# Kernel optimization log

Hardware: AMD Instinct MI355X
Metric: run time of the kernel (lower is better)

Reference implementation:

```python
import jax, jax.numpy as jnp
import numpy as np

N_NODES = 50000
N_EDGES = 500000
IN_CH = 128
OUT_CH = 128
N_TYPES = 2
NEG_SLOPE = 0.2
EPS = 1e-16


def setup_inputs() -> dict:
    key = jax.random.key(0)
    ks = jax.random.split(key, 8)
    x = jax.random.normal(ks[0], (N_NODES, IN_CH), dtype=jnp.float32)
    edge_index = jax.random.randint(ks[1], (2, N_EDGES), 0, N_NODES, dtype=jnp.int64)
    edge_type = jax.random.randint(ks[2], (N_EDGES,), 0, N_TYPES, dtype=jnp.int64)
    # xavier-uniform-like params
    def xav(k, shape, fan_in, fan_out):
        lim = np.sqrt(6.0 / (fan_in + fan_out)).astype(np.float32)
        return jax.random.uniform(k, shape, jnp.float32, -lim, lim)
    weight = xav(ks[3], (N_TYPES, IN_CH, OUT_CH), IN_CH, OUT_CH)
    att = xav(ks[4], (N_TYPES, 2 * OUT_CH), N_TYPES, 2 * OUT_CH)
    root_w = xav(ks[5], (OUT_CH, IN_CH), IN_CH, OUT_CH)
    lim = 1.0 / np.sqrt(IN_CH)
    root_b = jax.random.uniform(ks[6], (OUT_CH,), jnp.float32, -lim, lim)
    return {"x": x, "edge_index": edge_index, "edge_type": edge_type,
            "weight": weight, "att": att, "root_w": root_w, "root_b": root_b}


def reference(x, edge_index, edge_type, weight, att, root_w, root_b):
    n = x.shape[0]
    src, dst = edge_index[0], edge_index[1]
    # Per-edge transform x[src] @ W[edge_type] == gather from per-type node transforms
    h_all = jnp.einsum('ni,tio->nto', x, weight)          # [N, T, O]
    h_src = h_all[src, edge_type]                          # [E, O]
    h_dst = h_all[dst, edge_type]                          # [E, O]
    a = att[edge_type]                                     # [E, 2O]
    o = h_src.shape[1]
    e = (h_src * a[:, :o]).sum(-1) + (h_dst * a[:, o:]).sum(-1)
    e = jnp.where(e > 0, e, NEG_SLOPE * e)                 # leaky_relu
    # segment softmax over dst (stable: subtract per-segment max)
    seg_max = jax.ops.segment_max(e, dst, num_segments=n)
    ex = jnp.exp(e - seg_max[dst])
    denom = jax.ops.segment_sum(ex, dst, num_segments=n)
    alpha = ex / (denom[dst] + EPS)
    # dropout is identity in eval mode
    msg = h_src * alpha[:, None]
    out = jax.ops.segment_sum(msg, dst, num_segments=n)
    out = out + x @ root_w.T + root_b
    return out
```

## Files before the change

kernel.cpp:

```cpp
#include <hip/hip_runtime.h>
#include <hip/hip_bf16.h>

#define N_NODES 50000
#define N_EDGES 500000
#define IN_CH 128
#define OUT_CH 128
#define N_TYPES 2
#define NEG_SLOPE 0.2f
#define EPS_F 1e-16f

typedef __attribute__((ext_vector_type(8))) short bf16x8;
typedef __attribute__((ext_vector_type(4))) float f32x4;

__device__ __forceinline__ unsigned short bf16_rne(float f) {
    unsigned int u = __float_as_uint(f);
    u += 0x7FFFu + ((u >> 16) & 1u);
    return (unsigned short)(u >> 16);
}
__device__ __forceinline__ float bf16_to_f32(unsigned short h) {
    return __uint_as_float(((unsigned int)h) << 16);
}

__global__ __launch_bounds__(256) void bprep_kernel(
    const float* __restrict__ weight, const float* __restrict__ root_w,
    unsigned short* __restrict__ bt_hi, unsigned short* __restrict__ bt_lo)
{
    int i = blockIdx.x * 256 + threadIdx.x;
    if (i >= 384 * 128) return;
    int n = i >> 7, k = i & 127;
    float v;
    if (n < 256) {
        int t = n >> 7, o = n & 127;
        v = weight[(size_t)t * 16384 + (size_t)k * 128 + o];
    } else {
        v = root_w[(size_t)(n - 256) * 128 + k];
    }
    unsigned short h = bf16_rne(v);
    float lo = v - bf16_to_f32(h);
    bt_hi[i] = h;
    bt_lo[i] = bf16_rne(lo);
}

#define MBLK 391
#define LSWZ(row, col) ((row) * 128 + ((col) ^ (((row) & 7) << 3)))

__global__ __launch_bounds__(256, 2) void mfma_gemm_kernel(
    const float* __restrict__ x,
    const unsigned short* __restrict__ bt_hi,
    const unsigned short* __restrict__ bt_lo,
    const float* __restrict__ root_b,
    float* __restrict__ hall, float* __restrict__ out)
{
    __shared__ unsigned short Ah[128 * 128];
    __shared__ unsigned short Al[128 * 128];

    const int tid = threadIdx.x;
    const int bid = blockIdx.x;
    const int c = bid / MBLK;
    const int m0 = (bid - c * MBLK) * 128;

    {
        const float4* xg = (const float4*)x;
        #pragma unroll
        for (int it = 0; it < 16; ++it) {
            int idx = tid + it * 256;
            int r = idx >> 5, c4 = idx & 31;
            int gn = m0 + r;
            float4 v = make_float4(0.f, 0.f, 0.f, 0.f);
            if (gn < N_NODES) v = xg[(size_t)gn * 32 + c4];
            unsigned short h0 = bf16_rne(v.x), h1 = bf16_rne(v.y),
                           h2 = bf16_rne(v.z), h3 = bf16_rne(v.w);
            ushort4 hh = make_ushort4(h0, h1, h2, h3);
            ushort4 ll = make_ushort4(bf16_rne(v.x - bf16_to_f32(h0)),
                                      bf16_rne(v.y - bf16_to_f32(h1)),
                                      bf16_rne(v.z - bf16_to_f32(h2)),
                                      bf16_rne(v.w - bf16_to_f32(h3)));
            int off = LSWZ(r, c4 * 4);
            *(ushort4*)&Ah[off] = hh;
            *(ushort4*)&Al[off] = ll;
        }
    }
    __syncthreads();

    const int lane = tid & 63;
    const int w = tid >> 6;
    const int mh = (w >> 1) * 64;
    const int nh = (w & 1) * 64;
    const int lr = lane & 15;
    const int lk = (lane >> 4) * 8;

    const unsigned short* bh_base =
        bt_hi + ((size_t)(c * 128 + nh + lr)) * 128 + lk;
    const unsigned short* bl_base =
        bt_lo + ((size_t)(c * 128 + nh + lr)) * 128 + lk;

    f32x4 acc[4][4];
    #pragma unroll
    for (int mi = 0; mi < 4; ++mi)
        #pragma unroll
        for (int ni = 0; ni < 4; ++ni)
            acc[mi][ni] = (f32x4){0.f, 0.f, 0.f, 0.f};

    #pragma unroll
    for (int ks = 0; ks < 4; ++ks) {
        const int ko = ks * 32 + lk;
        bf16x8 bh[4], bl[4];
        #pragma unroll
        for (int ni = 0; ni < 4; ++ni) {
            bh[ni] = *(const bf16x8*)(bh_base + ni * 2048 + ks * 32);
            bl[ni] = *(const bf16x8*)(bl_base + ni * 2048 + ks * 32);
        }
        bf16x8 ah[4], al[4];
        #pragma unroll
        for (int mi = 0; mi < 4; ++mi) {
            int off = LSWZ(mh + mi * 16 + lr, ko);
            ah[mi] = *(const bf16x8*)&Ah[off];
            al[mi] = *(const bf16x8*)&Al[off];
        }
        #pragma unroll
        for (int mi = 0; mi < 4; ++mi)
            #pragma unroll
            for (int ni = 0; ni < 4; ++ni) {
                acc[mi][ni] = __builtin_amdgcn_mfma_f32_16x16x32_bf16(
                    ah[mi], bh[ni], acc[mi][ni], 0, 0, 0);
                acc[mi][ni] = __builtin_amdgcn_mfma_f32_16x16x32_bf16(
                    ah[mi], bl[ni], acc[mi][ni], 0, 0, 0);
                acc[mi][ni] = __builtin_amdgcn_mfma_f32_16x16x32_bf16(
                    al[mi], bh[ni], acc[mi][ni], 0, 0, 0);
            }
    }

    const int crow = (lane >> 4) * 4;
    const int ccol = lane & 15;
    if (c < 2) {
        #pragma unroll
        for (int mi = 0; mi < 4; ++mi)
            #pragma unroll
            for (int j = 0; j < 4; ++j) {
                int gm = m0 + mh + mi * 16 + crow + j;
                if (gm < N_NODES) {
                    #pragma unroll
                    for (int ni = 0; ni < 4; ++ni) {
                        int n = nh + ni * 16 + ccol;
                        hall[((size_t)gm * 2 + c) * 128 + n] = acc[mi][ni][j];
                    }
                }
            }
    } else {
        float rbv[4];
        #pragma unroll
        for (int ni = 0; ni < 4; ++ni) rbv[ni] = root_b[nh + ni * 16 + ccol];
        #pragma unroll
        for (int mi = 0; mi < 4; ++mi)
            #pragma unroll
            for (int j = 0; j < 4; ++j) {
                int gm = m0 + mh + mi * 16 + crow + j;
                if (gm < N_NODES) {
                    #pragma unroll
                    for (int ni = 0; ni < 4; ++ni) {
                        int n = nh + ni * 16 + ccol;
                        out[(size_t)gm * 128 + n] = acc[mi][ni][j] + rbv[ni];
                    }
                }
            }
    }
}

__global__ __launch_bounds__(256) void hist_kernel(
    const int* __restrict__ ei, int* __restrict__ deg)
{
    int i = blockIdx.x * 256 + threadIdx.x;
    if (i < N_EDGES) atomicAdd(&deg[ei[N_EDGES + i]], 1);
}

__global__ __launch_bounds__(256) void scan1_kernel(
    const int* __restrict__ deg, int* __restrict__ rp, int* __restrict__ bsum)
{
    __shared__ int s[256];
    int i = blockIdx.x * 256 + threadIdx.x;
    int v = (i < N_NODES) ? deg[i] : 0;
    s[threadIdx.x] = v;
    __syncthreads();
    #pragma unroll
    for (int off = 1; off < 256; off <<= 1) {
        int t = (threadIdx.x >= off) ? s[threadIdx.x - off] : 0;
        __syncthreads();
        s[threadIdx.x] += t;
        __syncthreads();
    }
    if (i < N_NODES) rp[i + 1] = s[threadIdx.x];
    if (threadIdx.x == 255) bsum[blockIdx.x] = s[255];
    if (i == 0) rp[0] = 0;
}

__global__ __launch_bounds__(256) void scan2_kernel(int* __restrict__ bsum, int nb)
{
    __shared__ int s[256];
    int tid = threadIdx.x;
    int v = (tid < nb) ? bsum[tid] : 0;
    s[tid] = v;
    __syncthreads();
    #pragma unroll
    for (int off = 1; off < 256; off <<= 1) {
        int t = (tid >= off) ? s[tid - off] : 0;
        __syncthreads();
        s[tid] += t;
        __syncthreads();
    }
    if (tid < nb) bsum[tid] = s[tid] - v;
}

__global__ __launch_bounds__(256) void scan3_kernel(
    int* __restrict__ rp, const int* __restrict__ bsum)
{
    int i = blockIdx.x * 256 + threadIdx.x;
    if (i < N_NODES) rp[i + 1] += bsum[blockIdx.x];
}

__global__ __launch_bounds__(256) void csr_scatter_kernel(
    const int* __restrict__ ei, const int* __restrict__ etype,
    const int* __restrict__ rp, int* __restrict__ cursor, int* __restrict__ skey)
{
    int i = blockIdx.x * 256 + threadIdx.x;
    if (i >= N_EDGES) return;
    int dst = ei[N_EDGES + i];
    int pos = rp[dst] + atomicAdd(&cursor[dst], 1);
    skey[pos] = (ei[i] << 1) | (etype[i] & 1);
}

__device__ __forceinline__ float dot4(float4 a, float4 b) {
    return a.x * b.x + a.y * b.y + a.z * b.z + a.w * b.w;
}

__global__ __launch_bounds__(256) void node_agg_kernel(
    const int* __restrict__ rp, const int* __restrict__ skey,
    const float* __restrict__ hall, const float* __restrict__ att,
    float* __restrict__ out)
{
    const int lane = threadIdx.x & 63;
    const int sl = lane & 31;
    const int half = lane >> 5;
    const int wid = (blockIdx.x * 256 + threadIdx.x) >> 6;
    const int node = wid * 2 + half;
    if (node >= N_NODES) return;
    const int row0 = rp[node], row1 = rp[node + 1];

    const float4 al0 = *(const float4*)&att[0 * 256 + sl * 4];
    const float4 ar0 = *(const float4*)&att[0 * 256 + 128 + sl * 4];
    const float4 al1 = *(const float4*)&att[1 * 256 + sl * 4];
    const float4 ar1 = *(const float4*)&att[1 * 256 + 128 + sl * 4];

    const float4 hd0 = *(const float4*)&hall[((size_t)node * 2 + 0) * 128 + sl * 4];
    const float4 hd1 = *(const float4*)&hall[((size_t)node * 2 + 1) * 128 + sl * 4];
    float dr0 = dot4(hd0, ar0);
    float dr1 = dot4(hd1, ar1);
    #pragma unroll
    for (int off = 16; off; off >>= 1) {
        dr0 += __shfl_xor(dr0, off);
        dr1 += __shfl_xor(dr1, off);
    }

    const float NINF = -__builtin_inff();
    float m = NINF, denom = 0.f;
    float4 acc = make_float4(0.f, 0.f, 0.f, 0.f);

    for (int j = row0; j < row1; j += 4) {
        const int je = row1 - 1;
        const int k0 = skey[j];
        const int k1 = skey[min(j + 1, je)];
        const int k2 = skey[min(j + 2, je)];
        const int k3 = skey[min(j + 3, je)];
        const int t0 = k0 & 1, t1 = k1 & 1, t2 = k2 & 1, t3 = k3 & 1;

        const float4 h0 = *(const float4*)&hall[((size_t)(k0 >> 1) * 2 + t0) * 128 + sl * 4];
        const float4 h1 = *(const float4*)&hall[((size_t)(k1 >> 1) * 2 + t1) * 128 + sl * 4];
        const float4 h2 = *(const float4*)&hall[((size_t)(k2 >> 1) * 2 + t2) * 128 + sl * 4];
        const float4 h3 = *(const float4*)&hall[((size_t)(k3 >> 1) * 2 + t3) * 128 + sl * 4];

        float p0 = dot4(h0, t0 ? al1 : al0);
        float p1 = dot4(h1, t1 ? al1 : al0);
        float p2 = dot4(h2, t2 ? al1 : al0);
        float p3 = dot4(h3, t3 ? al1 : al0);
        #pragma unroll
        for (int off = 16; off; off >>= 1) {
            p0 += __shfl_xor(p0, off);
            p1 += __shfl_xor(p1, off);
            p2 += __shfl_xor(p2, off);
            p3 += __shfl_xor(p3, off);
        }

        float e0 = p0 + (t0 ? dr1 : dr0);
        float e1 = p1 + (t1 ? dr1 : dr0);
        float e2 = p2 + (t2 ? dr1 : dr0);
        float e3 = p3 + (t3 ? dr1 : dr0);
        e0 = (e0 > 0.f) ? e0 : NEG_SLOPE * e0;
        e1 = (e1 > 0.f) ? e1 : NEG_SLOPE * e1;
        e2 = (e2 > 0.f) ? e2 : NEG_SLOPE * e2;
        e3 = (e3 > 0.f) ? e3 : NEG_SLOPE * e3;
        if (j + 1 > je) e1 = NINF;
        if (j + 2 > je) e2 = NINF;
        if (j + 3 > je) e3 = NINF;

        const float mx = fmaxf(fmaxf(e0, e1), fmaxf(e2, e3));
        const float mn = fmaxf(m, mx);
        const float r = __expf(m - mn);
        m = mn;
        const float w0 = __expf(e0 - m);
        const float w1 = __expf(e1 - m);
        const float w2 = __expf(e2 - m);
        const float w3 = __expf(e3 - m);
        denom = denom * r + (w0 + w1) + (w2 + w3);
        acc.x = acc.x * r + w0 * h0.x + w1 * h1.x + w2 * h2.x + w3 * h3.x;
        acc.y = acc.y * r + w0 * h0.y + w1 * h1.y + w2 * h2.y + w3 * h3.y;
        acc.z = acc.z * r + w0 * h0.z + w1 * h1.z + w2 * h2.z + w3 * h3.z;
        acc.w = acc.w * r + w0 * h0.w + w1 * h1.w + w2 * h2.w + w3 * h3.w;
    }

    if (row0 < row1) {
        const float inv = 1.f / (denom + EPS_F);
        float4* op = (float4*)&out[(size_t)node * 128 + sl * 4];
        float4 o = *op;
        o.x += acc.x * inv;
        o.y += acc.y * inv;
        o.z += acc.z * inv;
        o.w += acc.w * inv;
        *op = o;
    }
}

extern "C" void kernel_launch(void* const* d_in, const int* in_sizes, int n_in,
                              void* d_out, int out_size, void* d_ws, size_t ws_size,
                              hipStream_t stream) {
    const float* x      = (const float*)d_in[0];
    const int*   ei     = (const int*)d_in[1];
    const int*   etype  = (const int*)d_in[2];
    const float* weight = (const float*)d_in[3];
    const float* att    = (const float*)d_in[4];
    const float* root_w = (const float*)d_in[5];
    const float* root_b = (const float*)d_in[6];
    float* out = (float*)d_out;

    float* hall  = (float*)d_ws;
    int* deg     = (int*)(hall + (size_t)N_NODES * 2 * 128);
    int* cursor  = deg + N_NODES;
    int* rp      = cursor + N_NODES;
    int* bsum    = rp + (N_NODES + 1);
    int* skey    = bsum + 256;
    unsigned short* bt_hi = (unsigned short*)(skey + N_EDGES);
    unsigned short* bt_lo = bt_hi + 384 * 128;

    const int NB_E = (N_EDGES + 255) / 256;
    const int NB_N = (N_NODES + 255) / 256;

    hipMemsetAsync(deg, 0, sizeof(int) * (size_t)N_NODES * 2, stream);

    bprep_kernel<<<192, 256, 0, stream>>>(weight, root_w, bt_hi, bt_lo);

    mfma_gemm_kernel<<<3 * MBLK, 256, 0, stream>>>(
        x, bt_hi, bt_lo, root_b, hall, out);

    hist_kernel<<<NB_E, 256, 0, stream>>>(ei, deg);
    scan1_kernel<<<NB_N, 256, 0, stream>>>(deg, rp, bsum);
    scan2_kernel<<<1, 256, 0, stream>>>(bsum, NB_N);
    scan3_kernel<<<NB_N, 256, 0, stream>>>(rp, bsum);
    csr_scatter_kernel<<<NB_E, 256, 0, stream>>>(ei, etype, rp, cursor, skey);

    node_agg_kernel<<<(N_NODES + 7) / 8, 256, 0, stream>>>(
        rp, skey, hall, att, out);
}
```

Measured before the change: 240.8 us.

## Precompute attention scores in GEMM epilogue and use two-pass segment softmax

```diff
diff --git a/kernel.cpp b/kernel.cpp
--- a/kernel.cpp
+++ b/kernel.cpp
@@ -2,10 +2,10 @@
 #include <hip/hip_bf16.h>
 
 #define N_NODES 50000
+#define N_PAD 50048
 #define N_EDGES 500000
 #define IN_CH 128
 #define OUT_CH 128
-#define N_TYPES 2
 #define NEG_SLOPE 0.2f
 #define EPS_F 1e-16f
 
@@ -21,69 +21,92 @@
     return __uint_as_float(((unsigned int)h) << 16);
 }
 
-__global__ __launch_bounds__(256) void bprep_kernel(
-    const float* __restrict__ weight, const float* __restrict__ root_w,
+#define XSWZ(n, k) ((size_t)(n) * 128 + ((k) ^ (((n) & 7) << 3)))
+#define LSWZ(row, col) ((row) * 128 + ((col) ^ (((row) & 7) << 3)))
+
+__device__ __forceinline__ void gload16(const unsigned short* g, unsigned short* l) {
+    __builtin_amdgcn_global_load_lds(
+        (const __attribute__((address_space(1))) unsigned int*)g,
+        (__attribute__((address_space(3))) unsigned int*)l, 16, 0, 0);
+}
+
+__global__ __launch_bounds__(256) void prep_kernel(
+    const float* __restrict__ x, const float* __restrict__ weight,
+    const float* __restrict__ root_w,
+    unsigned short* __restrict__ xhi, unsigned short* __restrict__ xlo,
     unsigned short* __restrict__ bt_hi, unsigned short* __restrict__ bt_lo)
 {
-    int i = blockIdx.x * 256 + threadIdx.x;
-    if (i >= 384 * 128) return;
-    int n = i >> 7, k = i & 127;
-    float v;
-    if (n < 256) {
-        int t = n >> 7, o = n & 127;
-        v = weight[(size_t)t * 16384 + (size_t)k * 128 + o];
-    } else {
-        v = root_w[(size_t)(n - 256) * 128 + k];
-    }
-    unsigned short h = bf16_rne(v);
-    float lo = v - bf16_to_f32(h);
-    bt_hi[i] = h;
-    bt_lo[i] = bf16_rne(lo);
+    const int gid = blockIdx.x * 256 + threadIdx.x;
+    const int gsz = gridDim.x * 256;
+
+    const float4* xg = (const float4*)x;
+    for (int i = gid; i < N_PAD * 32; i += gsz) {
+        int n = i >> 5, c4 = i & 31;
+        float4 v = make_float4(0.f, 0.f, 0.f, 0.f);
+        if (n < N_NODES) v = xg[(size_t)n * 32 + c4];
+        unsigned short h0 = bf16_rne(v.x), h1 = bf16_rne(v.y),
+                       h2 = bf16_rne(v.z), h3 = bf16_rne(v.w);
+        ushort4 hh = make_ushort4(h0, h1, h2, h3);
+        ushort4 ll = make_ushort4(bf16_rne(v.x - bf16_to_f32(h0)),
+                                  bf16_rne(v.y - bf16_to_f32(h1)),
+                                  bf16_rne(v.z - bf16_to_f32(h2)),
+                                  bf16_rne(v.w - bf16_to_f32(h3)));
+        size_t off = XSWZ(n, c4 * 4);
+        *(ushort4*)&xhi[off] = hh;
+        *(ushort4*)&xlo[off] = ll;
+    }
+
+    for (int i = gid; i < 384 * 128; i += gsz) {
+        int n = i >> 7, k = i & 127;
+        float v;
+        if (n < 256) {
+            int t = n >> 7, o = n & 127;
+            v = weight[(size_t)t * 16384 + (size_t)k * 128 + o];
+        } else {
+            v = root_w[(size_t)(n - 256) * 128 + k];
+        }
+        unsigned short h = bf16_rne(v);
+        bt_hi[i] = h;
+        bt_lo[i] = bf16_rne(v - bf16_to_f32(h));
+    }
 }
 
 #define MBLK 391
-#define LSWZ(row, col) ((row) * 128 + ((col) ^ (((row) & 7) << 3)))
 
 __global__ __launch_bounds__(256, 2) void mfma_gemm_kernel(
-    const float* __restrict__ x,
+    const unsigned short* __restrict__ xhi,
+    const unsigned short* __restrict__ xlo,
     const unsigned short* __restrict__ bt_hi,
     const unsigned short* __restrict__ bt_lo,
-    const float* __restrict__ root_b,
-    float* __restrict__ hall, float* __restrict__ out)
+    const float* __restrict__ att, const float* __restrict__ root_b,
+    float* __restrict__ hall, float* __restrict__ out,
+    float* __restrict__ sL, float* __restrict__ sR)
 {
     __shared__ unsigned short Ah[128 * 128];
     __shared__ unsigned short Al[128 * 128];
+    __shared__ float sLds[128][2];
 
     const int tid = threadIdx.x;
+    const int lane = tid & 63;
+    const int w = tid >> 6;
     const int bid = blockIdx.x;
     const int c = bid / MBLK;
     const int m0 = (bid - c * MBLK) * 128;
 
+    if (tid < 128) { sLds[tid][0] = 0.f; sLds[tid][1] = 0.f; }
+
     {
-        const float4* xg = (const float4*)x;
-        #pragma unroll
-        for (int it = 0; it < 16; ++it) {
-            int idx = tid + it * 256;
-            int r = idx >> 5, c4 = idx & 31;
-            int gn = m0 + r;
-            float4 v = make_float4(0.f, 0.f, 0.f, 0.f);
-            if (gn < N_NODES) v = xg[(size_t)gn * 32 + c4];
-            unsigned short h0 = bf16_rne(v.x), h1 = bf16_rne(v.y),
-                           h2 = bf16_rne(v.z), h3 = bf16_rne(v.w);
-            ushort4 hh = make_ushort4(h0, h1, h2, h3);
-            ushort4 ll = make_ushort4(bf16_rne(v.x - bf16_to_f32(h0)),
-                                      bf16_rne(v.y - bf16_to_f32(h1)),
-                                      bf16_rne(v.z - bf16_to_f32(h2)),
-                                      bf16_rne(v.w - bf16_to_f32(h3)));
-            int off = LSWZ(r, c4 * 4);
-            *(ushort4*)&Ah[off] = hh;
-            *(ushort4*)&Al[off] = ll;
+        const unsigned short* srch = xhi + (size_t)m0 * 128;
+        const unsigned short* srcl = xlo + (size_t)m0 * 128;
+        #pragma unroll
+        for (int it = 0; it < 8; ++it) {
+            int base = it * 2048 + w * 512;
+            gload16(srch + base + lane * 8, &Ah[base]);
+            gload16(srcl + base + lane * 8, &Al[base]);
         }
     }
     __syncthreads();
 
-    const int lane = tid & 63;
-    const int w = tid >> 6;
     const int mh = (w >> 1) * 64;
     const int nh = (w & 1) * 64;
     const int lr = lane & 15;
@@ -146,6 +169,36 @@
                     }
                 }
             }
+        float attLv[4], attRv[4];
+        #pragma unroll
+        for (int ni = 0; ni < 4; ++ni) {
+            attLv[ni] = att[c * 256 + nh + ni * 16 + ccol];
+            attRv[ni] = att[c * 256 + 128 + nh + ni * 16 + ccol];
+        }
+        #pragma unroll
+        for (int mi = 0; mi < 4; ++mi)
+            #pragma unroll
+            for (int j = 0; j < 4; ++j) {
+                float pL = acc[mi][0][j] * attLv[0] + acc[mi][1][j] * attLv[1]
+                         + acc[mi][2][j] * attLv[2] + acc[mi][3][j] * attLv[3];
+                float pR = acc[mi][0][j] * attRv[0] + acc[mi][1][j] * attRv[1]
+                         + acc[mi][2][j] * attRv[2] + acc[mi][3][j] * attRv[3];
+                #pragma unroll
+                for (int off = 1; off < 16; off <<= 1) {
+                    pL += __shfl_xor(pL, off);
+                    pR += __shfl_xor(pR, off);
+                }
+                if (ccol == 0) {
+                    int rl = mh + mi * 16 + crow + j;
+                    atomicAdd(&sLds[rl][0], pL);
+                    atomicAdd(&sLds[rl][1], pR);
+                }
+            }
+        __syncthreads();
+        if (tid < 128) {
+            sL[(size_t)(m0 + tid) * 2 + c] = sLds[tid][0];
+            sR[(size_t)(m0 + tid) * 2 + c] = sLds[tid][1];
+        }
     } else {
         float rbv[4];
         #pragma unroll
@@ -193,28 +246,21 @@
     if (i == 0) rp[0] = 0;
 }
 
-__global__ __launch_bounds__(256) void scan2_kernel(int* __restrict__ bsum, int nb)
-{
-    __shared__ int s[256];
+__global__ __launch_bounds__(256) void scan23_kernel(
+    int* __restrict__ rp, const int* __restrict__ bsum, int nb)
+{
+    __shared__ int bl[256];
     int tid = threadIdx.x;
-    int v = (tid < nb) ? bsum[tid] : 0;
-    s[tid] = v;
+    bl[tid] = (tid < nb && tid < (int)blockIdx.x) ? bsum[tid] : 0;
     __syncthreads();
     #pragma unroll
-    for (int off = 1; off < 256; off <<= 1) {
-        int t = (tid >= off) ? s[tid - off] : 0;
+    for (int off = 128; off; off >>= 1) {
+        if (tid < off) bl[tid] += bl[tid + off];
         __syncthreads();
-        s[tid] += t;
-        __syncthreads();
-    }
-    if (tid < nb) bsum[tid] = s[tid] - v;
-}
-
-__global__ __launch_bounds__(256) void scan3_kernel(
-    int* __restrict__ rp, const int* __restrict__ bsum)
-{
-    int i = blockIdx.x * 256 + threadIdx.x;
-    if (i < N_NODES) rp[i + 1] += bsum[blockIdx.x];
+    }
+    int pre = bl[0];
+    int i = blockIdx.x * 256 + tid;
+    if (i < N_NODES) rp[i + 1] += pre;
 }
 
 __global__ __launch_bounds__(256) void csr_scatter_kernel(
@@ -228,95 +274,68 @@
     skey[pos] = (ei[i] << 1) | (etype[i] & 1);
 }
 
-__device__ __forceinline__ float dot4(float4 a, float4 b) {
-    return a.x * b.x + a.y * b.y + a.z * b.z + a.w * b.w;
-}
-
 __global__ __launch_bounds__(256) void node_agg_kernel(
     const int* __restrict__ rp, const int* __restrict__ skey,
-    const float* __restrict__ hall, const float* __restrict__ att,
+    const float* __restrict__ hall,
+    const float* __restrict__ sL, const float* __restrict__ sR,
     float* __restrict__ out)
 {
     const int lane = threadIdx.x & 63;
+    const int node = (blockIdx.x * 256 + threadIdx.x) >> 6;
+    if (node >= N_NODES) return;
+    const int r0 = rp[node], r1 = rp[node + 1];
+    if (r0 == r1) return;
+
+    const float sR0 = sR[(size_t)node * 2 + 0];
+    const float sR1 = sR[(size_t)node * 2 + 1];
+    const float NINF = -__builtin_inff();
+
+    float mloc = NINF;
+    for (int j = r0 + lane; j < r1; j += 64) {
+        int key = skey[j], t = key & 1;
+        float e = sL[(size_t)(key >> 1) * 2 + t] + (t ? sR1 : sR0);
+        e = (e > 0.f) ? e : NEG_SLOPE * e;
+        mloc = fmaxf(mloc, e);
+    }
+    #pragma unroll
+    for (int off = 32; off; off >>= 1) mloc = fmaxf(mloc, __shfl_xor(mloc, off));
+
     const int sl = lane & 31;
     const int half = lane >> 5;
-    const int wid = (blockIdx.x * 256 + threadIdx.x) >> 6;
-    const int node = wid * 2 + half;
-    if (node >= N_NODES) return;
-    const int row0 = rp[node], row1 = rp[node + 1];
-
-    const float4 al0 = *(const float4*)&att[0 * 256 + sl * 4];
-    const float4 ar0 = *(const float4*)&att[0 * 256 + 128 + sl * 4];
-    const float4 al1 = *(const float4*)&att[1 * 256 + sl * 4];
-    const float4 ar1 = *(const float4*)&att[1 * 256 + 128 + sl * 4];
-
-    const float4 hd0 = *(const float4*)&hall[((size_t)node * 2 + 0) * 128 + sl * 4];
-    const float4 hd1 = *(const float4*)&hall[((size_t)node * 2 + 1) * 128 + sl * 4];
-    float dr0 = dot4(hd0, ar0);
-    float dr1 = dot4(hd1, ar1);
-    #pragma unroll
-    for (int off = 16; off; off >>= 1) {
-        dr0 += __shfl_xor(dr0, off);
-        dr1 += __shfl_xor(dr1, off);
-    }
-
-    const float NINF = -__builtin_inff();
-    float m = NINF, denom = 0.f;
+    float denom = 0.f;
     float4 acc = make_float4(0.f, 0.f, 0.f, 0.f);
 
-    for (int j = row0; j < row1; j += 4) {
-        const int je = row1 - 1;
-        const int k0 = skey[j];
-        const int k1 = skey[min(j + 1, je)];
-        const int k2 = skey[min(j + 2, je)];
-        const int k3 = skey[min(j + 3, je)];
-        const int t0 = k0 & 1, t1 = k1 & 1, t2 = k2 & 1, t3 = k3 & 1;
-
-        const float4 h0 = *(const float4*)&hall[((size_t)(k0 >> 1) * 2 + t0) * 128 + sl * 4];
+    for (int j = r0 + half; j < r1; j += 4) {
+        const int j2 = j + 2;
+        const bool v2 = j2 < r1;
+        const int k1 = skey[j];
+        const int k2 = skey[v2 ? j2 : j];
+        const int t1 = k1 & 1, t2 = k2 & 1;
+
+        float e1 = sL[(size_t)(k1 >> 1) * 2 + t1] + (t1 ? sR1 : sR0);
+        float e2 = sL[(size_t)(k2 >> 1) * 2 + t2] + (t2 ? sR1 : sR0);
+        e1 = (e1 > 0.f) ? e1 : NEG_SLOPE * e1;
+        e2 = (e2 > 0.f) ? e2 : NEG_SLOPE * e2;
+        const float w1 = __expf(e1 - mloc);
+        const float w2 = v2 ? __expf(e2 - mloc) : 0.f;
+
         const float4 h1 = *(const float4*)&hall[((size_t)(k1 >> 1) * 2 + t1) * 128 + sl * 4];
         const float4 h2 = *(const float4*)&hall[((size_t)(k2 >> 1) * 2 + t2) * 128 + sl * 4];
-        const float4 h3 = *(const float4*)&hall[((size_t)(k3 >> 1) * 2 + t3) * 128 + sl * 4];
-
-        float p0 = dot4(h0, t0 ? al1 : al0);
-        float p1 = dot4(h1, t1 ? al1 : al0);
-        float p2 = dot4(h2, t2 ? al1 : al0);
-        float p3 = dot4(h3, t3 ? al1 : al0);
-        #pragma unroll
-        for (int off = 16; off; off >>= 1) {
-            p0 += __shfl_xor(p0, off);
-            p1 += __shfl_xor(p1, off);
-            p2 += __shfl_xor(p2, off);
-            p3 += __shfl_xor(p3, off);
-        }
-
-        float e0 = p0 + (t0 ? dr1 : dr0);
-        float e1 = p1 + (t1 ? dr1 : dr0);
-        float e2 = p2 + (t2 ? dr1 : dr0);
-        float e3 = p3 + (t3 ? dr1 : dr0);
-        e0 = (e0 > 0.f) ? e0 : NEG_SLOPE * e0;
-        e1 = (e1 > 0.f) ? e1 : NEG_SLOPE * e1;
-        e2 = (e2 > 0.f) ? e2 : NEG_SLOPE * e2;
-        e3 = (e3 > 0.f) ? e3 : NEG_SLOPE * e3;
-        if (j + 1 > je) e1 = NINF;
-        if (j + 2 > je) e2 = NINF;
-        if (j + 3 > je) e3 = NINF;
-
-        const float mx = fmaxf(fmaxf(e0, e1), fmaxf(e2, e3));
-        const float mn = fmaxf(m, mx);
-        const float r = __expf(m - mn);
-        m = mn;
-        const float w0 = __expf(e0 - m);
-        const float w1 = __expf(e1 - m);
-        const float w2 = __expf(e2 - m);
-        const float w3 = __expf(e3 - m);
-        denom = denom * r + (w0 + w1) + (w2 + w3);
-        acc.x = acc.x * r + w0 * h0.x + w1 * h1.x + w2 * h2.x + w3 * h3.x;
-        acc.y = acc.y * r + w0 * h0.y + w1 * h1.y + w2 * h2.y + w3 * h3.y;
-        acc.z = acc.z * r + w0 * h0.z + w1 * h1.z + w2 * h2.z + w3 * h3.z;
-        acc.w = acc.w * r + w0 * h0.w + w1 * h1.w + w2 * h2.w + w3 * h3.w;
-    }
-
-    if (row0 < row1) {
+
+        denom += w1 + w2;
+        acc.x += w1 * h1.x + w2 * h2.x;
+        acc.y += w1 * h1.y + w2 * h2.y;
+        acc.z += w1 * h1.z + w2 * h2.z;
+        acc.w += w1 * h1.w + w2 * h2.w;
+    }
+
+    denom += __shfl_xor(denom, 32);
+    acc.x += __shfl_xor(acc.x, 32);
+    acc.y += __shfl_xor(acc.y, 32);
+    acc.z += __shfl_xor(acc.z, 32);
+    acc.w += __shfl_xor(acc.w, 32);
+
+    if (half == 0) {
         const float inv = 1.f / (denom + EPS_F);
         float4* op = (float4*)&out[(size_t)node * 128 + sl * 4];
         float4 o = *op;
@@ -340,31 +359,35 @@
     const float* root_b = (const float*)d_in[6];
     float* out = (float*)d_out;
 
-    float* hall  = (float*)d_ws;
-    int* deg     = (int*)(hall + (size_t)N_NODES * 2 * 128);
-    int* cursor  = deg + N_NODES;
-    int* rp      = cursor + N_NODES;
-    int* bsum    = rp + (N_NODES + 1);
-    int* skey    = bsum + 256;
-    unsigned short* bt_hi = (unsigned short*)(skey + N_EDGES);
+    float* ws = (float*)d_ws;
+    float* hall   = ws;
+    float* sL     = hall + (size_t)N_NODES * 2 * 128;
+    float* sR     = sL + (size_t)N_PAD * 2;
+    int*   deg    = (int*)(sR + (size_t)N_PAD * 2);
+    int*   cursor = deg + N_PAD;
+    int*   rp     = cursor + N_PAD;
+    int*   bsum   = rp + 50056;
+    int*   skey   = bsum + 256;
+    unsigned short* xhi   = (unsigned short*)(skey + N_EDGES);
+    unsigned short* xlo   = xhi + (size_t)N_PAD * 128;
+    unsigned short* bt_hi = xlo + (size_t)N_PAD * 128;
     unsigned short* bt_lo = bt_hi + 384 * 128;
 
     const int NB_E = (N_EDGES + 255) / 256;
     const int NB_N = (N_NODES + 255) / 256;
 
-    hipMemsetAsync(deg, 0, sizeof(int) * (size_t)N_NODES * 2, stream);
-
-    bprep_kernel<<<192, 256, 0, stream>>>(weight, root_w, bt_hi, bt_lo);
+    hipMemsetAsync(deg, 0, sizeof(int) * (size_t)N_PAD * 2, stream);
+
+    prep_kernel<<<2048, 256, 0, stream>>>(x, weight, root_w, xhi, xlo, bt_hi, bt_lo);
 
     mfma_gemm_kernel<<<3 * MBLK, 256, 0, stream>>>(
-        x, bt_hi, bt_lo, root_b, hall, out);
+        xhi, xlo, bt_hi, bt_lo, att, root_b, hall, out, sL, sR);
 
     hist_kernel<<<NB_E, 256, 0, stream>>>(ei, deg);
     scan1_kernel<<<NB_N, 256, 0, stream>>>(deg, rp, bsum);
-    scan2_kernel<<<1, 256, 0, stream>>>(bsum, NB_N);
-    scan3_kernel<<<NB_N, 256, 0, stream>>>(rp, bsum);
+    scan23_kernel<<<NB_N, 256, 0, stream>>>(rp, bsum, NB_N);
     csr_scatter_kernel<<<NB_E, 256, 0, stream>>>(ei, etype, rp, cursor, skey);
 
-    node_agg_kernel<<<(N_NODES + 7) / 8, 256, 0, stream>>>(
-        rp, skey, hall, att, out);
-}
+    node_agg_kernel<<<(N_NODES + 3) / 4, 256, 0, stream>>>(
+        rp, skey, hall, sL, sR, out);
+}
```

Result: no change. 243.5 us (+1.1%).
